# Performance work log

Measured on AMD Instinct MI355X. Metric: run time of the kernel, lower is better.

The kernel has to match this reference:

```python
import jax, jax.numpy as jnp
import numpy as np

N = 8192
IN_F = 512
OUT_F = 512
ALPHA = 0.2  # leaky relu slope


def setup_inputs() -> dict:
    key = jax.random.key(0)
    k1, k2, k3, k4, k5 = jax.random.split(key, 5)
    inp = jax.random.normal(k1, (N, IN_F), dtype=jnp.float32)
    adj = jax.random.randint(k2, (N, N), 0, 2, dtype=jnp.int32)
    # linear1: [in, out] + bias
    W1 = jax.random.normal(k3, (IN_F, OUT_F), dtype=jnp.float32) * (1.0 / np.sqrt(IN_F))
    b1 = jnp.zeros((OUT_F,), dtype=jnp.float32)
    # linear2: maps 2*out -> 1; split into the two halves acting on h_i and h_j
    a = jax.random.normal(k4, (2 * OUT_F,), dtype=jnp.float32) * (1.0 / np.sqrt(2 * OUT_F))
    a1 = a[:OUT_F]
    a2 = a[OUT_F:]
    b2 = jnp.zeros((), dtype=jnp.float32)
    return {"inp": inp, "adj": adj, "W1": W1, "b1": b1, "a1": a1, "a2": a2, "b2": b2}


def reference(inp, adj, W1, b1, a1, a2, b2):
    h = inp @ W1 + b1  # [N, out]
    # linear2(cat(h_i, h_j)) == h_i@a1 + h_j@a2 + b2 -> avoids the N*N*2F tensor
    e = jax.nn.leaky_relu((h @ a1)[:, None] + (h @ a2)[None, :] + b2, ALPHA)  # [N, N]
    attention = jnp.where(adj > 0, e, jnp.float32(-1e12))
    attention = jax.nn.softmax(attention, axis=1)
    h_prime = attention @ h  # [N, out]
    return jax.nn.elu(h_prime)  # concat=True
```

## Files before the change

kernel.cpp:

```cpp
#include <hip/hip_runtime.h>
#include <hip/hip_bf16.h>
#include <stdint.h>

#define NR 8192
#define FD 512
#define BM 64
#define PADC 36

typedef __attribute__((ext_vector_type(8))) short s8v;
typedef __attribute__((ext_vector_type(4))) float f32x4;

static __device__ __forceinline__ short bf16_rtne(float x) {
    union { float f; uint32_t u; } v; v.f = x;
    uint32_t r = (v.u + 0x7FFFu + ((v.u >> 16) & 1u)) >> 16;
    return (short)r;
}
static __device__ __forceinline__ float bf16_to_f32(short s) {
    union { uint32_t u; float f; } v; v.u = ((uint32_t)(uint16_t)s) << 16;
    return v.f;
}

__global__ void k_prepack(const int* __restrict__ adj,
                          unsigned long long* __restrict__ bm) {
    const int lane = threadIdx.x & 63;
    const int wv   = threadIdx.x >> 6;
    const int gid  = blockIdx.x * 4 + wv;
    const int row  = gid >> 2;
    const int seg  = (gid & 3) * 2048;
    const int* p   = adj + (size_t)row * NR + seg + lane;
    unsigned long long* o = bm + (((size_t)row * NR + seg) >> 6);
#pragma unroll
    for (int g = 0; g < 8; ++g) {
        unsigned long long b0 = __ballot(p[g * 256]       != 0);
        unsigned long long b1 = __ballot(p[g * 256 + 64]  != 0);
        unsigned long long b2 = __ballot(p[g * 256 + 128] != 0);
        unsigned long long b3 = __ballot(p[g * 256 + 192] != 0);
        unsigned long long vs = (lane == 0) ? b0 : (lane == 1) ? b1
                              : (lane == 2) ? b2 : b3;
        if (lane < 4) o[g * 4 + lane] = vs;
    }
}

__global__ void k_convert(const float* __restrict__ in, short* __restrict__ out) {
    int i = blockIdx.x * blockDim.x + threadIdx.x;
    float4 v = ((const float4*)in)[i];
    short4 s;
    s.x = bf16_rtne(v.x); s.y = bf16_rtne(v.y);
    s.z = bf16_rtne(v.z); s.w = bf16_rtne(v.w);
    ((short4*)out)[i] = s;
}

__global__ void k_w1t(const float* __restrict__ W1, short* __restrict__ W1T) {
    int i = blockIdx.x * 256 + threadIdx.x;
    int k = i & 511, n = i >> 9;
    W1T[(size_t)n * 512 + k] = bf16_rtne(W1[(size_t)k * 512 + n]);
}

__launch_bounds__(256)
__global__ void k_gemm_h(const short* __restrict__ A,
                         const short* __restrict__ BT,
                         const float* __restrict__ b1,
                         short* __restrict__ H,
                         short* __restrict__ HT36)
{
    const int lane = threadIdx.x & 63;
    const int wn   = threadIdx.x >> 6;
    const int m    = lane & 15;
    const int q    = lane >> 4;
    const int r0   = blockIdx.x * 32;
    const int c0   = blockIdx.y * 128 + wn * 32;

    f32x4 acc[2][2] = {};
#pragma unroll 1
    for (int k0 = 0; k0 < 512; k0 += 32) {
        s8v a[2], b[2];
#pragma unroll
        for (int rt = 0; rt < 2; ++rt)
            a[rt] = *(const s8v*)(A + (size_t)(r0 + rt * 16 + m) * 512 + k0 + q * 8);
#pragma unroll
        for (int nt = 0; nt < 2; ++nt)
            b[nt] = *(const s8v*)(BT + (size_t)(c0 + nt * 16 + m) * 512 + k0 + q * 8);
#pragma unroll
        for (int rt = 0; rt < 2; ++rt)
#pragma unroll
            for (int nt = 0; nt < 2; ++nt)
                acc[rt][nt] = __builtin_amdgcn_mfma_f32_16x16x32_bf16(a[rt], b[nt], acc[rt][nt], 0, 0, 0);
    }
    float b1v[2];
#pragma unroll
    for (int nt = 0; nt < 2; ++nt) b1v[nt] = b1[c0 + nt * 16 + m];

#pragma unroll
    for (int rt = 0; rt < 2; ++rt)
#pragma unroll
        for (int nt = 0; nt < 2; ++nt) {
            int col = c0 + nt * 16 + m;
            short4 hp;
#pragma unroll
            for (int r = 0; r < 4; ++r) {
                int row = r0 + rt * 16 + q * 4 + r;
                short hv = bf16_rtne(acc[rt][nt][r] + b1v[nt]);
                H[(size_t)row * 512 + col] = hv;
                ((short*)&hp)[r] = hv;
            }
            *(short4*)(HT36 + (size_t)blockIdx.x * (512 * PADC)
                             + (size_t)col * PADC + rt * 16 + q * 4) = hp;
        }
}

__global__ void k_f1f2(const short* __restrict__ H, const float* __restrict__ a1,
                       const float* __restrict__ a2, const float* __restrict__ b2,
                       float* __restrict__ f1, float* __restrict__ f2s)
{
    const int lane = threadIdx.x & 63;
    const int row  = blockIdx.x * 4 + (threadIdx.x >> 6);
    s8v hv = *(const s8v*)(H + (size_t)row * 512 + lane * 8);
    float4 a1l = ((const float4*)(a1 + lane * 8))[0];
    float4 a1h = ((const float4*)(a1 + lane * 8))[1];
    float4 a2l = ((const float4*)(a2 + lane * 8))[0];
    float4 a2h = ((const float4*)(a2 + lane * 8))[1];
    float hf[8];
#pragma unroll
    for (int i = 0; i < 8; ++i) hf[i] = bf16_to_f32(hv[i]);
    float s1 = hf[0] * a1l.x + hf[1] * a1l.y + hf[2] * a1l.z + hf[3] * a1l.w
             + hf[4] * a1h.x + hf[5] * a1h.y + hf[6] * a1h.z + hf[7] * a1h.w;
    float s2 = hf[0] * a2l.x + hf[1] * a2l.y + hf[2] * a2l.z + hf[3] * a2l.w
             + hf[4] * a2h.x + hf[5] * a2h.y + hf[6] * a2h.z + hf[7] * a2h.w;
#pragma unroll
    for (int o = 32; o > 0; o >>= 1) {
        s1 += __shfl_xor(s1, o);
        s2 += __shfl_xor(s2, o);
    }
    if (lane == 0) {
        f1[row]  = s1;
        f2s[row] = s2 + b2[0];
    }
}

__launch_bounds__(512, 4)
__global__ void k_attn(const uint32_t* __restrict__ bm,
                       const short* __restrict__ HT36,
                       const float* __restrict__ f1,
                       const float* __restrict__ f2s,
                       float* __restrict__ nump,
                       float* __restrict__ denomp)
{
    __shared__ __align__(16) short bbuf[2][512 * PADC];
    __shared__ __align__(16) short wt[2][BM * 32];

    const int t    = threadIdx.x;
    const int lane = t & 63;
    const int w    = t >> 6;
    const int m    = lane & 15;
    const int q    = lane >> 4;

    const int js   = blockIdx.x & 3;
    const int band = blockIdx.x >> 2;
    const int r0   = band * BM;
    const int jb0  = js * 2048;

    const int prow = t >> 3;
    const int jg   = t & 7;

    const float f1v = f1[r0 + prow];
    const uint32_t* bmrow = bm + (size_t)(r0 + prow) * 256 + js * 64;
    const float*    f2p   = f2s + jb0 + jg * 4;

    f32x4 acc[4][4] = {};
    float dsum = 0.f;

#define GAT_DMA(KT, PN)                                                        \
    {                                                                          \
        const short* srcb = HT36 + (size_t)(js * 64 + (KT)) * (512 * PADC);    \
        short* dstb = &bbuf[PN][0];                                            \
        _Pragma("unroll")                                                      \
        for (int r_ = 0; r_ < 5; ++r_) {                                       \
            int g_ = w + 8 * r_;                                               \
            if (g_ < 36) {                                                     \
                __builtin_amdgcn_global_load_lds(                              \
                    (const __attribute__((address_space(1))) int*)             \
                        (srcb + g_ * 512 + lane * 8),                          \
                    (__attribute__((address_space(3))) int*)(dstb + g_ * 512), \
                    16, 0, 0);                                                 \
            }                                                                  \
        }                                                                      \
    }

#define GAT_WGEN(KT, PN)                                                       \
    {                                                                          \
        uint32_t wd_ = bmrow[KT];                                              \
        float4 f2_ = *(const float4*)(f2p + (KT) * 32);                        \
        uint32_t nib_ = wd_ >> (jg * 4);                                       \
        short4 sv_;                                                            \
        _Pragma("unroll")                                                      \
        for (int jj = 0; jj < 4; ++jj) {                                       \
            float s_ = f1v + ((const float*)&f2_)[jj];                         \
            float e_ = __expf(fmaxf(s_, 0.2f * s_));                           \
            float x_ = ((nib_ >> jj) & 1u) ? e_ : 0.f;                         \
            dsum += x_;                                                        \
            ((short*)&sv_)[jj] = bf16_rtne(x_);                                \
        }                                                                      \
        *(short4*)&wt[PN][prow * 32 + (((jg >> 1) ^ (prow & 3)) << 3)          \
                          + (jg & 1) * 4] = sv_;                               \
    }

    GAT_DMA(0, 0)
    GAT_WGEN(0, 0)
    __syncthreads();

#pragma unroll 1
    for (int kk = 0; kk < 64; ++kk) {
        const int p = kk & 1;
        const bool more = (kk < 63);

        if (more) GAT_DMA(kk + 1, p ^ 1)

        s8v af[4];
#pragma unroll
        for (int i = 0; i < 4; ++i)
            af[i] = *(const s8v*)&wt[p][(i * 16 + m) * 32 + ((q ^ (m & 3)) << 3)];
        const short* bb = &bbuf[p][0];
#pragma unroll
        for (int nt = 0; nt < 4; ++nt) {
            int col = w * 64 + nt * 16 + m;
            union { short4 h[2]; s8v v; } bu;
            bu.h[0] = *(const short4*)&bb[col * PADC + q * 8];
            bu.h[1] = *(const short4*)&bb[col * PADC + q * 8 + 4];
#pragma unroll
            for (int i = 0; i < 4; ++i)
                acc[i][nt] = __builtin_amdgcn_mfma_f32_16x16x32_bf16(af[i], bu.v, acc[i][nt], 0, 0, 0);
        }

        if (more) GAT_WGEN(kk + 1, p ^ 1)

        __syncthreads();
    }
#undef GAT_DMA
#undef GAT_WGEN

    dsum += __shfl_xor(dsum, 1);
    dsum += __shfl_xor(dsum, 2);
    dsum += __shfl_xor(dsum, 4);
    if (jg == 0) denomp[(size_t)js * NR + r0 + prow] = dsum;

    float* np = nump + (size_t)js * NR * FD;
#pragma unroll
    for (int i = 0; i < 4; ++i)
#pragma unroll
        for (int nt = 0; nt < 4; ++nt)
#pragma unroll
            for (int r = 0; r < 4; ++r) {
                int row = r0 + i * 16 + q * 4 + r;
                int col = w * 64 + nt * 16 + m;
                np[(size_t)row * FD + col] = acc[i][nt][r];
            }
}

__global__ void k_combine(const float* __restrict__ nump,
                          const float* __restrict__ denomp,
                          float* __restrict__ out)
{
    size_t e = ((size_t)blockIdx.x * 256 + threadIdx.x) * 4;
    int row = (int)(e >> 9);
    float4 n0 = *(const float4*)(nump + e);
    float4 n1 = *(const float4*)(nump + (size_t)NR * FD + e);
    float4 n2 = *(const float4*)(nump + (size_t)2 * NR * FD + e);
    float4 n3 = *(const float4*)(nump + (size_t)3 * NR * FD + e);
    float d = denomp[row] + denomp[NR + row] + denomp[2 * NR + row] + denomp[3 * NR + row];
    float inv = 1.0f / d;
    float4 o;
    o.x = (n0.x + n1.x + n2.x + n3.x) * inv;
    o.y = (n0.y + n1.y + n2.y + n3.y) * inv;
    o.z = (n0.z + n1.z + n2.z + n3.z) * inv;
    o.w = (n0.w + n1.w + n2.w + n3.w) * inv;
    o.x = (o.x > 0.f) ? o.x : (__expf(o.x) - 1.f);
    o.y = (o.y > 0.f) ? o.y : (__expf(o.y) - 1.f);
    o.z = (o.z > 0.f) ? o.z : (__expf(o.z) - 1.f);
    o.w = (o.w > 0.f) ? o.w : (__expf(o.w) - 1.f);
    *(float4*)(out + e) = o;
}

extern "C" void kernel_launch(void* const* d_in, const int* in_sizes, int n_in,
                              void* d_out, int out_size, void* d_ws, size_t ws_size,
                              hipStream_t stream) {
    const float* inp = (const float*)d_in[0];
    const int*   adj = (const int*)d_in[1];
    const float* W1  = (const float*)d_in[2];
    const float* b1  = (const float*)d_in[3];
    const float* a1  = (const float*)d_in[4];
    const float* a2  = (const float*)d_in[5];
    const float* b2  = (const float*)d_in[6];
    float* out = (float*)d_out;

    short*    inp_bf = (short*)d_ws;
    short*    w1t    = inp_bf + (size_t)NR * FD;
    short*    h      = w1t + (size_t)FD * FD;
    short*    ht36   = h + (size_t)NR * FD;
    uint32_t* bmw    = (uint32_t*)(ht36 + (size_t)256 * 512 * PADC);
    float*    f1     = (float*)(bmw + (size_t)NR * 256);
    float*    f2s    = f1 + NR;
    float*    nump   = f2s + NR;
    float*    denomp = nump + (size_t)4 * NR * FD;

    k_prepack<<<NR, 256, 0, stream>>>(adj, (unsigned long long*)bmw);
    k_convert<<<(NR * FD / 4) / 256, 256, 0, stream>>>(inp, inp_bf);
    k_w1t<<<(FD * FD) / 256, 256, 0, stream>>>(W1, w1t);
    dim3 g1(NR / 32, FD / 128);
    k_gemm_h<<<g1, 256, 0, stream>>>(inp_bf, w1t, b1, h, ht36);
    k_f1f2<<<NR / 4, 256, 0, stream>>>(h, a1, a2, b2, f1, f2s);
    k_attn<<<128 * 4, 512, 0, stream>>>(bmw, ht36, f1, f2s, nump, denomp);
    k_combine<<<(NR * FD / 4) / 256, 256, 0, stream>>>(nump, denomp, out);
}
```

Baseline: 525.8 us.

## Restructure attention kernel with per-wave B staging and chunked weight generation

The attention kernel now splits the neighbor dimension in two instead of four, halving the partial numerator traffic written and re-read by the combine kernel. Each wave DMAs its own 64-column slice of H^T into a private double buffer, waiting only on its own memory counter rather than a block barrier. Attention weights are generated for 256 neighbors at a time, so there is one barrier per 8 k-tiles. The price is a larger LDS footprint, occupancy lowered to 2 blocks per CU, and only 256 blocks, which is about one wave of blocks across the device.

```diff
diff --git a/kernel.cpp b/kernel.cpp
--- a/kernel.cpp
+++ b/kernel.cpp
@@ -5,7 +5,6 @@
 #define NR 8192
 #define FD 512
 #define BM 64
-#define PADC 36
 
 typedef __attribute__((ext_vector_type(8))) short s8v;
 typedef __attribute__((ext_vector_type(4))) float f32x4;
@@ -61,7 +60,7 @@
                          const short* __restrict__ BT,
                          const float* __restrict__ b1,
                          short* __restrict__ H,
-                         short* __restrict__ HT36)
+                         short* __restrict__ HT2)
 {
     const int lane = threadIdx.x & 63;
     const int wn   = threadIdx.x >> 6;
@@ -103,8 +102,7 @@
                 H[(size_t)row * 512 + col] = hv;
                 ((short*)&hp)[r] = hv;
             }
-            *(short4*)(HT36 + (size_t)blockIdx.x * (512 * PADC)
-                             + (size_t)col * PADC + rt * 16 + q * 4) = hp;
+            *(short4*)(HT2 + (size_t)blockIdx.x * (512 * 32) + (size_t)col * 32 + rt * 16 + q * 4) = hp;
         }
 }
 
@@ -137,16 +135,16 @@
     }
 }
 
-__launch_bounds__(512, 4)
+__launch_bounds__(512, 2)
 __global__ void k_attn(const uint32_t* __restrict__ bm,
-                       const short* __restrict__ HT36,
+                       const short* __restrict__ HT2,
                        const float* __restrict__ f1,
                        const float* __restrict__ f2s,
                        float* __restrict__ nump,
                        float* __restrict__ denomp)
 {
-    __shared__ __align__(16) short bbuf[2][512 * PADC];
-    __shared__ __align__(16) short wt[2][BM * 32];
+    __shared__ __align__(16) short wt[2][BM * 256];
+    __shared__ __align__(16) short bbuf[8][2][2048];
 
     const int t    = threadIdx.x;
     const int lane = t & 63;
@@ -154,85 +152,97 @@
     const int m    = lane & 15;
     const int q    = lane >> 4;
 
-    const int js   = blockIdx.x & 3;
-    const int band = blockIdx.x >> 2;
+    const int js   = blockIdx.x & 1;
+    const int band = blockIdx.x >> 1;
     const int r0   = band * BM;
-    const int jb0  = js * 2048;
+    const int jb0  = js * 4096;
+    const int jt0  = js * 128;
 
     const int prow = t >> 3;
     const int jg   = t & 7;
 
     const float f1v = f1[r0 + prow];
-    const uint32_t* bmrow = bm + (size_t)(r0 + prow) * 256 + js * 64;
-    const float*    f2p   = f2s + jb0 + jg * 4;
+    const uint32_t* bmrow = bm + (size_t)(r0 + prow) * 256 + js * 128;
+    const float* f2base = f2s + jb0;
 
     f32x4 acc[4][4] = {};
     float dsum = 0.f;
 
-#define GAT_DMA(KT, PN)                                                        \
+#define GAT_DMA(KT)                                                            \
     {                                                                          \
-        const short* srcb = HT36 + (size_t)(js * 64 + (KT)) * (512 * PADC);    \
-        short* dstb = &bbuf[PN][0];                                            \
+        const short* src_ = HT2 + (size_t)(jt0 + (KT)) * (512 * 32) + w * 2048;\
+        short* dst_ = &bbuf[w][(KT) & 1][0];                                   \
         _Pragma("unroll")                                                      \
-        for (int r_ = 0; r_ < 5; ++r_) {                                       \
-            int g_ = w + 8 * r_;                                               \
-            if (g_ < 36) {                                                     \
-                __builtin_amdgcn_global_load_lds(                              \
-                    (const __attribute__((address_space(1))) int*)             \
-                        (srcb + g_ * 512 + lane * 8),                          \
-                    (__attribute__((address_space(3))) int*)(dstb + g_ * 512), \
-                    16, 0, 0);                                                 \
+        for (int b_ = 0; b_ < 4; ++b_) {                                       \
+            __builtin_amdgcn_global_load_lds(                                  \
+                (const __attribute__((address_space(1))) int*)                 \
+                    (src_ + b_ * 512 + lane * 8),                              \
+                (__attribute__((address_space(3))) int*)(dst_ + b_ * 512),     \
+                16, 0, 0);                                                     \
+        }                                                                      \
+    }
+
+#define GAT_WGEN(CH, P)                                                        \
+    {                                                                          \
+        uint4 mwa_ = *(const uint4*)(bmrow + (CH) * 8);                        \
+        uint4 mwb_ = *(const uint4*)(bmrow + (CH) * 8 + 4);                    \
+        uint32_t m8_[8] = {mwa_.x, mwa_.y, mwa_.z, mwa_.w,                     \
+                           mwb_.x, mwb_.y, mwb_.z, mwb_.w};                    \
+        _Pragma("unroll")                                                      \
+        for (int k_ = 0; k_ < 4; ++k_) {                                       \
+            const int u_ = jg + 8 * k_;                                        \
+            uint32_t byte_ = (m8_[(jg >> 2) + 2 * k_] >> ((jg & 3) * 8)) & 0xFFu; \
+            float4 fa_ = *(const float4*)(f2base + (CH) * 256 + u_ * 8);       \
+            float4 fb_ = *(const float4*)(f2base + (CH) * 256 + u_ * 8 + 4);   \
+            s8v wv_;                                                           \
+            const float* ff_ = (const float*)&fa_;                             \
+            _Pragma("unroll")                                                  \
+            for (int jj = 0; jj < 4; ++jj) {                                   \
+                float s_ = f1v + ff_[jj];                                      \
+                float e_ = __expf(fmaxf(s_, 0.2f * s_));                       \
+                float x_ = ((byte_ >> jj) & 1u) ? e_ : 0.f;                    \
+                dsum += x_; wv_[jj] = bf16_rtne(x_);                           \
             }                                                                  \
+            const float* fg_ = (const float*)&fb_;                            \
+            _Pragma("unroll")                                                  \
+            for (int jj = 0; jj < 4; ++jj) {                                   \
+                float s_ = f1v + fg_[jj];                                      \
+                float e_ = __expf(fmaxf(s_, 0.2f * s_));                       \
+                float x_ = ((byte_ >> (4 + jj)) & 1u) ? e_ : 0.f;              \
+                dsum += x_; wv_[4 + jj] = bf16_rtne(x_);                       \
+            }                                                                  \
+            *(s8v*)&wt[P][prow * 256 + ((u_ ^ (prow & 7)) << 3)] = wv_;        \
         }                                                                      \
     }
 
-#define GAT_WGEN(KT, PN)                                                       \
-    {                                                                          \
-        uint32_t wd_ = bmrow[KT];                                              \
-        float4 f2_ = *(const float4*)(f2p + (KT) * 32);                        \
-        uint32_t nib_ = wd_ >> (jg * 4);                                       \
-        short4 sv_;                                                            \
-        _Pragma("unroll")                                                      \
-        for (int jj = 0; jj < 4; ++jj) {                                       \
-            float s_ = f1v + ((const float*)&f2_)[jj];                         \
-            float e_ = __expf(fmaxf(s_, 0.2f * s_));                           \
-            float x_ = ((nib_ >> jj) & 1u) ? e_ : 0.f;                         \
-            dsum += x_;                                                        \
-            ((short*)&sv_)[jj] = bf16_rtne(x_);                                \
-        }                                                                      \
-        *(short4*)&wt[PN][prow * 32 + (((jg >> 1) ^ (prow & 3)) << 3)          \
-                          + (jg & 1) * 4] = sv_;                               \
-    }
-
-    GAT_DMA(0, 0)
+    GAT_DMA(0)
     GAT_WGEN(0, 0)
     __syncthreads();
 
+    int kt = 0;
 #pragma unroll 1
-    for (int kk = 0; kk < 64; ++kk) {
-        const int p = kk & 1;
-        const bool more = (kk < 63);
-
-        if (more) GAT_DMA(kk + 1, p ^ 1)
-
-        s8v af[4];
-#pragma unroll
-        for (int i = 0; i < 4; ++i)
-            af[i] = *(const s8v*)&wt[p][(i * 16 + m) * 32 + ((q ^ (m & 3)) << 3)];
-        const short* bb = &bbuf[p][0];
-#pragma unroll
-        for (int nt = 0; nt < 4; ++nt) {
-            int col = w * 64 + nt * 16 + m;
-            union { short4 h[2]; s8v v; } bu;
-            bu.h[0] = *(const short4*)&bb[col * PADC + q * 8];
-            bu.h[1] = *(const short4*)&bb[col * PADC + q * 8 + 4];
+    for (int ch = 0; ch < 16; ++ch) {
+        const int p = ch & 1;
+#pragma unroll
+        for (int kk = 0; kk < 8; ++kk, ++kt) {
+            const int bufc = kt & 1;
+            GAT_DMA((kt + 1) & 127)
+            __builtin_amdgcn_s_waitcnt(0x0F74);
+            s8v af[4];
 #pragma unroll
             for (int i = 0; i < 4; ++i)
-                acc[i][nt] = __builtin_amdgcn_mfma_f32_16x16x32_bf16(af[i], bu.v, acc[i][nt], 0, 0, 0);
+                af[i] = *(const s8v*)&wt[p][(i * 16 + m) * 256
+                                            + (((kk * 4 + q) ^ (m & 7)) << 3)];
+            const short* bb = &bbuf[w][bufc][0];
+#pragma unroll
+            for (int nt = 0; nt < 4; ++nt) {
+                s8v b = *(const s8v*)&bb[(nt * 16 + m) * 32 + q * 8];
+#pragma unroll
+                for (int i = 0; i < 4; ++i)
+                    acc[i][nt] = __builtin_amdgcn_mfma_f32_16x16x32_bf16(af[i], b, acc[i][nt], 0, 0, 0);
+            }
         }
-
-        if (more) GAT_WGEN(kk + 1, p ^ 1)
-
+        if (ch < 15) GAT_WGEN(ch + 1, p ^ 1)
         __syncthreads();
     }
 #undef GAT_DMA
@@ -264,15 +274,13 @@
     int row = (int)(e >> 9);
     float4 n0 = *(const float4*)(nump + e);
     float4 n1 = *(const float4*)(nump + (size_t)NR * FD + e);
-    float4 n2 = *(const float4*)(nump + (size_t)2 * NR * FD + e);
-    float4 n3 = *(const float4*)(nump + (size_t)3 * NR * FD + e);
-    float d = denomp[row] + denomp[NR + row] + denomp[2 * NR + row] + denomp[3 * NR + row];
+    float d = denomp[row] + denomp[NR + row];
     float inv = 1.0f / d;
     float4 o;
-    o.x = (n0.x + n1.x + n2.x + n3.x) * inv;
-    o.y = (n0.y + n1.y + n2.y + n3.y) * inv;
-    o.z = (n0.z + n1.z + n2.z + n3.z) * inv;
-    o.w = (n0.w + n1.w + n2.w + n3.w) * inv;
+    o.x = (n0.x + n1.x) * inv;
+    o.y = (n0.y + n1.y) * inv;
+    o.z = (n0.z + n1.z) * inv;
+    o.w = (n0.w + n1.w) * inv;
     o.x = (o.x > 0.f) ? o.x : (__expf(o.x) - 1.f);
     o.y = (o.y > 0.f) ? o.y : (__expf(o.y) - 1.f);
     o.z = (o.z > 0.f) ? o.z : (__expf(o.z) - 1.f);
@@ -295,19 +303,19 @@
     short*    inp_bf = (short*)d_ws;
     short*    w1t    = inp_bf + (size_t)NR * FD;
     short*    h      = w1t + (size_t)FD * FD;
-    short*    ht36   = h + (size_t)NR * FD;
-    uint32_t* bmw    = (uint32_t*)(ht36 + (size_t)256 * 512 * PADC);
+    short*    ht2    = h + (size_t)NR * FD;
+    uint32_t* bmw    = (uint32_t*)(ht2 + (size_t)FD * NR);
     float*    f1     = (float*)(bmw + (size_t)NR * 256);
     float*    f2s    = f1 + NR;
     float*    nump   = f2s + NR;
-    float*    denomp = nump + (size_t)4 * NR * FD;
+    float*    denomp = nump + (size_t)2 * NR * FD;
 
     k_prepack<<<NR, 256, 0, stream>>>(adj, (unsigned long long*)bmw);
     k_convert<<<(NR * FD / 4) / 256, 256, 0, stream>>>(inp, inp_bf);
     k_w1t<<<(FD * FD) / 256, 256, 0, stream>>>(W1, w1t);
     dim3 g1(NR / 32, FD / 128);
-    k_gemm_h<<<g1, 256, 0, stream>>>(inp_bf, w1t, b1, h, ht36);
+    k_gemm_h<<<g1, 256, 0, stream>>>(inp_bf, w1t, b1, h, ht2);
     k_f1f2<<<NR / 4, 256, 0, stream>>>(h, a1, a2, b2, f1, f2s);
-    k_attn<<<128 * 4, 512, 0, stream>>>(bmw, ht36, f1, f2s, nump, denomp);
+    k_attn<<<128 * 2, 512, 0, stream>>>(bmw, ht2, f1, f2s, nump, denomp);
     k_combine<<<(NR * FD / 4) / 256, 256, 0, stream>>>(nump, denomp, out);
 }
```

Result: no change. 515.8 us (-1.9%).
